# Kernel tuning notes

Measured on AMD Instinct MI355X. Metric: run time of the kernel, lower is better.

## Reference

```python
import jax, jax.numpy as jnp
import numpy as np

NUM_IT = 3

def squash(s):
    # squash along last (caps_dim) axis: |s|^2/(1+|s|^2) * s/|s|
    sq = jnp.sum(s * s, axis=-1, keepdims=True)
    return sq / (1.0 + sq) * (s / jnp.sqrt(sq))

def setup_inputs() -> dict:
    key = jax.random.key(0)
    k1, k2 = jax.random.split(key)
    prim_caps = jax.random.normal(k1, (256, 1152, 8), dtype=jnp.float32)
    W = jax.random.normal(k2, (1, 1152, 10, 16, 8), dtype=jnp.float32)
    return {"prim_caps": prim_caps, "W": W}

def reference(prim_caps, W):
    # u_hat[b,r,c,d] = W[0,r,c,d,i] @ prim_caps[b,r,i]
    u_hat = jnp.einsum('rcdi,bri->brcd', W[0], prim_caps)
    R, C = W.shape[1], W.shape[2]
    b_ij = jnp.zeros((R, C), dtype=u_hat.dtype)  # logits shared across batch
    v = None
    for _ in range(NUM_IT):
        c_ij = jax.nn.softmax(b_ij, axis=1)                     # softmax over caps dim
        s = jnp.einsum('rc,brcd->bcd', c_ij, u_hat)             # weighted sum over routes
        v = squash(s)                                            # [b, caps, dim]
        # agreement <u_hat, v>, averaged over batch (matches torch mean(dim=0))
        b_ij = b_ij + jnp.einsum('brcd,bcd->brc', u_hat, v).mean(axis=0)
    return v[..., None]  # [bs, num_caps, caps_dim, 1] matching torch output
```

## Files before the change

kernel.cpp:

```cpp
#include <hip/hip_runtime.h>
#include <hip/hip_bf16.h>
#include <math.h>


typedef __bf16 bf16x8 __attribute__((ext_vector_type(8)));
typedef float v4f __attribute__((ext_vector_type(4)));

__device__ __forceinline__ float b2f(unsigned short u) {
    return __uint_as_float(((unsigned)u) << 16);
}
__device__ __forceinline__ unsigned short f2b(float f) {
    unsigned x = __float_as_uint(f);
    return (unsigned short)((x + 0x7FFFu + ((x >> 16) & 1u)) >> 16);
}
__device__ __forceinline__ void split4(float4 x, unsigned short* h, unsigned short* l) {
    const float* xf = (const float*)&x;
    #pragma unroll
    for (int i = 0; i < 4; ++i) {
        h[i] = f2b(xf[i]);
        l[i] = f2b(xf[i] - b2f(h[i]));
    }
}
__device__ __forceinline__ uint2 pack4(const unsigned short* s) {
    uint2 w;
    w.x = s[0] | ((unsigned)s[1] << 16);
    w.y = s[2] | ((unsigned)s[3] << 16);
    return w;
}
__device__ __forceinline__ uint4 pack8(const unsigned short* s) {
    uint4 w;
    w.x = s[0] | ((unsigned)s[1] << 16); w.y = s[2] | ((unsigned)s[3] << 16);
    w.z = s[4] | ((unsigned)s[5] << 16); w.w = s[6] | ((unsigned)s[7] << 16);
    return w;
}

__global__ __launch_bounds__(256) void split_pw_kernel(
    const float4* __restrict__ P4, uint4* __restrict__ PAh, uint4* __restrict__ PAl,
    uint4* __restrict__ Pth, uint4* __restrict__ Ptl,
    const float4* __restrict__ W4, uint2* __restrict__ Wh, uint2* __restrict__ Wl)
{
    __shared__ unsigned short ldsH[64 * 72];
    __shared__ unsigned short ldsL[64 * 72];
    const int tid = threadIdx.x;

    if (blockIdx.x >= 576) {
        const int idx = (blockIdx.x - 576) * 256 + tid;
        unsigned short h[4], l[4];
        split4(W4[idx], h, l);
        Wh[idx] = pack4(h);
        Wl[idx] = pack4(l);
        return;
    }

    const int b0 = (blockIdx.x & 3) * 64;
    const int k0 = (blockIdx.x >> 2) * 64;
    #pragma unroll
    for (int j = 0; j < 4; ++j) {
        int idx = tid + j * 256;
        int row = idx >> 4, col4 = idx & 15;
        int g = (b0 + row) * 2304 + (k0 >> 2) + col4;
        unsigned short h[4], l[4];
        split4(P4[g], h, l);
        #pragma unroll
        for (int i = 0; i < 4; ++i) {
            ldsH[(col4 * 4 + i) * 72 + row] = h[i];
            ldsL[(col4 * 4 + i) * 72 + row] = l[i];
        }
    }
    __syncthreads();
    #pragma unroll
    for (int j = 0; j < 2; ++j) {
        int idx = tid + j * 256;
        int lane = idx & 63, sub = idx >> 6;
        int bt = sub & 3, kkl = sub >> 1 >> 1;
        int lm = lane & 15, q = lane >> 4;
        unsigned short h[8], l[8];
        #pragma unroll
        for (int t = 0; t < 8; ++t) {
            int kl = kkl * 32 + q * 8 + t;
            int row = bt * 16 + lm;
            h[t] = ldsH[kl * 72 + row];
            l[t] = ldsL[kl * 72 + row];
        }
        size_t o = ((size_t)((blockIdx.x & 3) * 4 + bt) * 288
                    + ((blockIdx.x >> 2) * 2 + kkl)) * 64 + lane;
        PAh[o] = pack8(h);
        PAl[o] = pack8(l);
    }
    #pragma unroll
    for (int j = 0; j < 2; ++j) {
        int idx = tid + j * 256;
        int krow = idx >> 3, bcol = idx & 7;
        unsigned short h[8], l[8];
        #pragma unroll
        for (int i = 0; i < 8; ++i) {
            h[i] = ldsH[krow * 72 + bcol * 8 + i];
            l[i] = ldsL[krow * 72 + bcol * 8 + i];
        }
        Pth[(size_t)(k0 + krow) * 32 + (b0 >> 3) + bcol] = pack8(h);
        Ptl[(size_t)(k0 + krow) * 32 + (b0 >> 3) + bcol] = pack8(l);
    }
}

__global__ __launch_bounds__(512) void sgemm_kernel(
    const uint4* __restrict__ Ah, const uint4* __restrict__ Al,
    const uint4* __restrict__ Bh, const uint4* __restrict__ Bl,
    uint2* __restrict__ vth, uint2* __restrict__ vtl,
    float* __restrict__ outb, int uniform, int last)
{
    __shared__ float comb[8][64][4];
    const int tid = threadIdx.x;
    const int wave = tid >> 6, lane = tid & 63;
    const int lm = lane & 15, q = lane >> 4;
    const int xcd = blockIdx.x & 7, s0 = blockIdx.x >> 3;
    const int c = (xcd & 1) * 5 + (s0 % 5);
    const int b0 = ((xcd >> 1) * 4 + (s0 / 5)) * 16;

    const uint4* Ahp = Ah + (size_t)(b0 >> 4) * 288 * 64 + lane;
    const uint4* Alp = Al + (size_t)(b0 >> 4) * 288 * 64 + lane;
    const uint4* Bhp = Bh + ((size_t)q * 10 + c) * 16 + lm;
    const uint4* Blp = Bl + ((size_t)q * 10 + c) * 16 + lm;

    v4f acc = {0.f, 0.f, 0.f, 0.f};
    const int kk0 = wave * 36;
    for (int kk = kk0; kk < kk0 + 36; ++kk) {
        bf16x8 ah = __builtin_bit_cast(bf16x8, Ahp[(size_t)kk * 64]);
        bf16x8 al = __builtin_bit_cast(bf16x8, Alp[(size_t)kk * 64]);
        bf16x8 bh = __builtin_bit_cast(bf16x8, Bhp[(size_t)kk * 640]);
        bf16x8 bl = __builtin_bit_cast(bf16x8, Blp[(size_t)kk * 640]);
        acc = __builtin_amdgcn_mfma_f32_16x16x32_bf16(ah, bh, acc, 0, 0, 0);
        acc = __builtin_amdgcn_mfma_f32_16x16x32_bf16(ah, bl, acc, 0, 0, 0);
        acc = __builtin_amdgcn_mfma_f32_16x16x32_bf16(al, bh, acc, 0, 0, 0);
    }
    #pragma unroll
    for (int r = 0; r < 4; ++r) comb[wave][lane][r] = acc[r];
    __syncthreads();
    if (wave == 0) {
        float s[4], sq[4];
        #pragma unroll
        for (int r = 0; r < 4; ++r) {
            s[r] = 0.f;
            #pragma unroll
            for (int w = 0; w < 8; ++w) s[r] += comb[w][lane][r];
            if (uniform) s[r] *= 0.1f;
            sq[r] = s[r] * s[r];
        }
        #pragma unroll
        for (int m = 1; m < 16; m <<= 1) {
            #pragma unroll
            for (int r = 0; r < 4; ++r) sq[r] += __shfl_xor(sq[r], m);
        }
        float v[4];
        #pragma unroll
        for (int r = 0; r < 4; ++r) {
            const float n = sq[r];
            v[r] = s[r] * sqrtf(n) / (1.0f + n);
        }
        if (!last) {
            unsigned short h[4], l[4];
            #pragma unroll
            for (int r = 0; r < 4; ++r) {
                h[r] = f2b(v[r]);
                l[r] = f2b(v[r] - b2f(h[r]));
            }
            const int o = (c * 16 + lm) * 64 + (b0 >> 2) + q;
            vth[o] = pack4(h);
            vtl[o] = pack4(l);
        } else {
            #pragma unroll
            for (int r = 0; r < 4; ++r)
                outb[((b0 + q * 4 + r) * 10 + c) * 16 + lm] = v[r];
        }
    }
}

__global__ __launch_bounds__(256) void agree_kernel(
    const uint4* __restrict__ vth, const uint4* __restrict__ vtl,
    const uint4* __restrict__ Pth, const uint4* __restrict__ Ptl,
    const float* __restrict__ Wf, float* __restrict__ b_log,
    unsigned short* __restrict__ Bh, unsigned short* __restrict__ Bl, int first)
{
    __shared__ float comb2[40][4][64];
    __shared__ float G_lds[160][18];
    __shared__ float part[4][10];
    __shared__ float cl[2][10];
    const int tid = threadIdx.x;
    const int wave = tid >> 6, lane = tid & 63;
    const int lm = lane & 15, q = lane >> 4;
    const int n0 = blockIdx.x * 16;

    v4f acc[10];
    #pragma unroll
    for (int mt = 0; mt < 10; ++mt) acc[mt] = (v4f){0.f, 0.f, 0.f, 0.f};
    #pragma unroll
    for (int kx = 0; kx < 2; ++kx) {
        const int kk = wave * 2 + kx;
        bf16x8 bh_ = __builtin_bit_cast(bf16x8, Pth[(size_t)(n0 + lm) * 32 + kk * 4 + q]);
        bf16x8 bl_ = __builtin_bit_cast(bf16x8, Ptl[(size_t)(n0 + lm) * 32 + kk * 4 + q]);
        #pragma unroll
        for (int mt = 0; mt < 10; ++mt) {
            bf16x8 ah = __builtin_bit_cast(bf16x8, vth[(size_t)(mt * 16 + lm) * 32 + kk * 4 + q]);
            bf16x8 al = __builtin_bit_cast(bf16x8, vtl[(size_t)(mt * 16 + lm) * 32 + kk * 4 + q]);
            acc[mt] = __builtin_amdgcn_mfma_f32_16x16x32_bf16(ah, bh_, acc[mt], 0, 0, 0);
            acc[mt] = __builtin_amdgcn_mfma_f32_16x16x32_bf16(ah, bl_, acc[mt], 0, 0, 0);
            acc[mt] = __builtin_amdgcn_mfma_f32_16x16x32_bf16(al, bh_, acc[mt], 0, 0, 0);
        }
    }
    #pragma unroll
    for (int mt = 0; mt < 10; ++mt)
        #pragma unroll
        for (int r = 0; r < 4; ++r)
            comb2[mt * 4 + r][wave][lane] = acc[mt][r];
    __syncthreads();
    #pragma unroll
    for (int j = 0; j < 10; ++j) {
        const int c40 = wave * 10 + j;
        float s_ = comb2[c40][0][lane] + comb2[c40][1][lane]
                 + comb2[c40][2][lane] + comb2[c40][3][lane];
        const int mt = c40 >> 2, reg = c40 & 3;
        G_lds[mt * 16 + q * 4 + reg][lm] = s_;
    }
    __syncthreads();

    const int rl = tid >> 7;
    const int t = tid & 127;
    const int r = (n0 >> 3) + rl;
    const int wid2 = tid >> 6;

    float wv[10], a[10];
    #pragma unroll
    for (int c = 0; c < 10; ++c) {
        wv[c] = Wf[((size_t)r * 10 + c) * 128 + t];
        float g = G_lds[c * 16 + (t >> 3)][rl * 8 + (t & 7)];
        a[c] = wv[c] * g;
    }
    #pragma unroll
    for (int m = 1; m < 64; m <<= 1) {
        #pragma unroll
        for (int c = 0; c < 10; ++c) a[c] += __shfl_xor(a[c], m);
    }
    if (lane == 0) {
        #pragma unroll
        for (int c = 0; c < 10; ++c) part[wid2][c] = a[c];
    }
    __syncthreads();
    if (t < 10) {
        float s_ = (part[rl * 2][t] + part[rl * 2 + 1][t]) * (1.0f / 256.0f);
        float bn = (first ? 0.f : b_log[r * 10 + t]) + s_;
        b_log[r * 10 + t] = bn;
        part[rl * 2][t] = bn;
    }
    __syncthreads();
    if (t < 10) {
        float mx = part[rl * 2][0];
        #pragma unroll
        for (int j = 1; j < 10; ++j) mx = fmaxf(mx, part[rl * 2][j]);
        float den = 0.f;
        #pragma unroll
        for (int j = 0; j < 10; ++j) den += __expf(part[rl * 2][j] - mx);
        cl[rl][t] = __expf(part[rl * 2][t] - mx) / den;
    }
    __syncthreads();
    #pragma unroll
    for (int c = 0; c < 10; ++c) {
        float x = cl[rl][c] * wv[c];
        unsigned short h = f2b(x);
        Bh[((size_t)r * 10 + c) * 128 + t] = h;
        Bl[((size_t)r * 10 + c) * 128 + t] = f2b(x - b2f(h));
    }
}

extern "C" void kernel_launch(void* const* d_in, const int* in_sizes, int n_in,
                              void* d_out, int out_size, void* d_ws, size_t ws_size,
                              hipStream_t stream)
{
    const float4* P4 = (const float4*)d_in[0];
    const float4* W4 = (const float4*)d_in[1];
    char* wsb = (char*)d_ws;
    float* b_log = (float*)(wsb + 0);
    uint2* vth   = (uint2*)(wsb + 131072);
    uint2* vtl   = (uint2*)(wsb + 262144);
    uint4* PAh   = (uint4*)(wsb + 393216);
    uint4* PAl   = (uint4*)(wsb + 5242880);
    uint4* Pth   = (uint4*)(wsb + 10485760);
    uint4* Ptl   = (uint4*)(wsb + 15728640);
    uint2* Wh    = (uint2*)(wsb + 20971520);
    uint2* Wl    = (uint2*)(wsb + 25165824);
    unsigned short* Bh = (unsigned short*)(wsb + 29360128);
    unsigned short* Bl = (unsigned short*)(wsb + 33554432);
    float* outb  = (float*)d_out;
    const float* Wf = (const float*)W4;

    split_pw_kernel<<<2016, 256, 0, stream>>>(P4, PAh, PAl, Pth, Ptl, W4, Wh, Wl);

    sgemm_kernel<<<160, 512, 0, stream>>>((const uint4*)PAh, (const uint4*)PAl,
                                          (const uint4*)Wh, (const uint4*)Wl,
                                          vth, vtl, outb, 1, 0);
    agree_kernel<<<576, 256, 0, stream>>>((const uint4*)vth, (const uint4*)vtl,
                                          Pth, Ptl, Wf, b_log, Bh, Bl, 1);
    sgemm_kernel<<<160, 512, 0, stream>>>((const uint4*)PAh, (const uint4*)PAl,
                                          (const uint4*)Bh, (const uint4*)Bl,
                                          vth, vtl, outb, 0, 0);
    agree_kernel<<<576, 256, 0, stream>>>((const uint4*)vth, (const uint4*)vtl,
                                          Pth, Ptl, Wf, b_log, Bh, Bl, 0);
    sgemm_kernel<<<160, 512, 0, stream>>>((const uint4*)PAh, (const uint4*)PAl,
                                          (const uint4*)Bh, (const uint4*)Bl,
                                          vth, vtl, outb, 0, 1);
}
```

Measured before the change: 160.5 us.

## Store MFMA operands in fragment-native layout for coalesced per-lane loads

Rewrites the layouts of W split, P transpose, v, and routing-weight buffers so that each MFMA operand fragment is a contiguous 64-lane block of uint4s. The sgemm and agree kernels then load B and A fragments with stride-64 lane-contiguous addresses instead of strided gathers. Producers (split kernel, sgemm epilogue, agree epilogue) write in the new tiled order, which makes some of their stores more scattered. The goal is to cut memory transactions in the hot GEMM loops.

```diff
diff --git a/kernel.cpp b/kernel.cpp
--- a/kernel.cpp
+++ b/kernel.cpp
@@ -36,7 +36,7 @@
 
 __global__ __launch_bounds__(256) void split_pw_kernel(
     const float4* __restrict__ P4, uint4* __restrict__ PAh, uint4* __restrict__ PAl,
-    uint4* __restrict__ Pth, uint4* __restrict__ Ptl,
+    uint4* __restrict__ PTh, uint4* __restrict__ PTl,
     const float4* __restrict__ W4, uint2* __restrict__ Wh, uint2* __restrict__ Wl)
 {
     __shared__ unsigned short ldsH[64 * 72];
@@ -45,10 +45,16 @@
 
     if (blockIdx.x >= 576) {
         const int idx = (blockIdx.x - 576) * 256 + tid;
+        const int j = idx & 1;
+        const int t16 = idx >> 1;
+        const int d = t16 & 15;
+        const int rc = t16 >> 4;
+        const int cc = rc % 10, r = rc / 10;
         unsigned short h[4], l[4];
         split4(W4[idx], h, l);
-        Wh[idx] = pack4(h);
-        Wl[idx] = pack4(l);
+        const size_t f = ((size_t)cc * 288 + (r >> 2)) * 64 + (r & 3) * 16 + d;
+        Wh[f * 2 + j] = pack4(h);
+        Wl[f * 2 + j] = pack4(l);
         return;
     }
 
@@ -72,7 +78,7 @@
     for (int j = 0; j < 2; ++j) {
         int idx = tid + j * 256;
         int lane = idx & 63, sub = idx >> 6;
-        int bt = sub & 3, kkl = sub >> 1 >> 1;
+        int bt = sub & 3, kkl = sub >> 2;
         int lm = lane & 15, q = lane >> 4;
         unsigned short h[8], l[8];
         #pragma unroll
@@ -97,8 +103,12 @@
             h[i] = ldsH[krow * 72 + bcol * 8 + i];
             l[i] = ldsL[krow * 72 + bcol * 8 + i];
         }
-        Pth[(size_t)(k0 + krow) * 32 + (b0 >> 3) + bcol] = pack8(h);
-        Ptl[(size_t)(k0 + krow) * 32 + (b0 >> 3) + bcol] = pack8(l);
+        const int gk = k0 + krow;
+        const int gcol = (b0 >> 3) + bcol;
+        const int kk = gcol >> 2, q = gcol & 3;
+        size_t o = ((size_t)(gk >> 4) * 8 + kk) * 64 + q * 16 + (gk & 15);
+        PTh[o] = pack8(h);
+        PTl[o] = pack8(l);
     }
 }
 
@@ -118,16 +128,16 @@
 
     const uint4* Ahp = Ah + (size_t)(b0 >> 4) * 288 * 64 + lane;
     const uint4* Alp = Al + (size_t)(b0 >> 4) * 288 * 64 + lane;
-    const uint4* Bhp = Bh + ((size_t)q * 10 + c) * 16 + lm;
-    const uint4* Blp = Bl + ((size_t)q * 10 + c) * 16 + lm;
+    const uint4* Bhp = Bh + (size_t)c * 288 * 64 + lane;
+    const uint4* Blp = Bl + (size_t)c * 288 * 64 + lane;
 
     v4f acc = {0.f, 0.f, 0.f, 0.f};
     const int kk0 = wave * 36;
     for (int kk = kk0; kk < kk0 + 36; ++kk) {
         bf16x8 ah = __builtin_bit_cast(bf16x8, Ahp[(size_t)kk * 64]);
         bf16x8 al = __builtin_bit_cast(bf16x8, Alp[(size_t)kk * 64]);
-        bf16x8 bh = __builtin_bit_cast(bf16x8, Bhp[(size_t)kk * 640]);
-        bf16x8 bl = __builtin_bit_cast(bf16x8, Blp[(size_t)kk * 640]);
+        bf16x8 bh = __builtin_bit_cast(bf16x8, Bhp[(size_t)kk * 64]);
+        bf16x8 bl = __builtin_bit_cast(bf16x8, Blp[(size_t)kk * 64]);
         acc = __builtin_amdgcn_mfma_f32_16x16x32_bf16(ah, bh, acc, 0, 0, 0);
         acc = __builtin_amdgcn_mfma_f32_16x16x32_bf16(ah, bl, acc, 0, 0, 0);
         acc = __builtin_amdgcn_mfma_f32_16x16x32_bf16(al, bh, acc, 0, 0, 0);
@@ -163,9 +173,11 @@
                 h[r] = f2b(v[r]);
                 l[r] = f2b(v[r] - b2f(h[r]));
             }
-            const int o = (c * 16 + lm) * 64 + (b0 >> 2) + q;
-            vth[o] = pack4(h);
-            vtl[o] = pack4(l);
+            const int jcol = (b0 >> 2) + q;
+            const int J = jcol >> 1;
+            const size_t f = ((size_t)c * 8 + (J >> 2)) * 64 + (J & 3) * 16 + lm;
+            vth[f * 2 + (jcol & 1)] = pack4(h);
+            vtl[f * 2 + (jcol & 1)] = pack4(l);
         } else {
             #pragma unroll
             for (int r = 0; r < 4; ++r)
@@ -176,7 +188,7 @@
 
 __global__ __launch_bounds__(256) void agree_kernel(
     const uint4* __restrict__ vth, const uint4* __restrict__ vtl,
-    const uint4* __restrict__ Pth, const uint4* __restrict__ Ptl,
+    const uint4* __restrict__ PTh, const uint4* __restrict__ PTl,
     const float* __restrict__ Wf, float* __restrict__ b_log,
     unsigned short* __restrict__ Bh, unsigned short* __restrict__ Bl, int first)
 {
@@ -189,18 +201,23 @@
     const int lm = lane & 15, q = lane >> 4;
     const int n0 = blockIdx.x * 16;
 
+    const uint4* PThp = PTh + (size_t)blockIdx.x * 512 + lane;
+    const uint4* PTlp = PTl + (size_t)blockIdx.x * 512 + lane;
+    const uint4* vthp = vth + lane;
+    const uint4* vtlp = vtl + lane;
+
     v4f acc[10];
     #pragma unroll
     for (int mt = 0; mt < 10; ++mt) acc[mt] = (v4f){0.f, 0.f, 0.f, 0.f};
     #pragma unroll
     for (int kx = 0; kx < 2; ++kx) {
         const int kk = wave * 2 + kx;
-        bf16x8 bh_ = __builtin_bit_cast(bf16x8, Pth[(size_t)(n0 + lm) * 32 + kk * 4 + q]);
-        bf16x8 bl_ = __builtin_bit_cast(bf16x8, Ptl[(size_t)(n0 + lm) * 32 + kk * 4 + q]);
+        bf16x8 bh_ = __builtin_bit_cast(bf16x8, PThp[(size_t)kk * 64]);
+        bf16x8 bl_ = __builtin_bit_cast(bf16x8, PTlp[(size_t)kk * 64]);
         #pragma unroll
         for (int mt = 0; mt < 10; ++mt) {
-            bf16x8 ah = __builtin_bit_cast(bf16x8, vth[(size_t)(mt * 16 + lm) * 32 + kk * 4 + q]);
-            bf16x8 al = __builtin_bit_cast(bf16x8, vtl[(size_t)(mt * 16 + lm) * 32 + kk * 4 + q]);
+            bf16x8 ah = __builtin_bit_cast(bf16x8, vthp[(size_t)(mt * 8 + kk) * 64]);
+            bf16x8 al = __builtin_bit_cast(bf16x8, vtlp[(size_t)(mt * 8 + kk) * 64]);
             acc[mt] = __builtin_amdgcn_mfma_f32_16x16x32_bf16(ah, bh_, acc[mt], 0, 0, 0);
             acc[mt] = __builtin_amdgcn_mfma_f32_16x16x32_bf16(ah, bl_, acc[mt], 0, 0, 0);
             acc[mt] = __builtin_amdgcn_mfma_f32_16x16x32_bf16(al, bh_, acc[mt], 0, 0, 0);
@@ -265,8 +282,9 @@
     for (int c = 0; c < 10; ++c) {
         float x = cl[rl][c] * wv[c];
         unsigned short h = f2b(x);
-        Bh[((size_t)r * 10 + c) * 128 + t] = h;
-        Bl[((size_t)r * 10 + c) * 128 + t] = f2b(x - b2f(h));
+        const size_t base = ((size_t)c * 288 + (r >> 2)) * 512 + 128 * (r & 3);
+        Bh[base + t] = h;
+        Bl[base + t] = f2b(x - b2f(h));
     }
 }
 
@@ -282,8 +300,8 @@
     uint2* vtl   = (uint2*)(wsb + 262144);
     uint4* PAh   = (uint4*)(wsb + 393216);
     uint4* PAl   = (uint4*)(wsb + 5242880);
-    uint4* Pth   = (uint4*)(wsb + 10485760);
-    uint4* Ptl   = (uint4*)(wsb + 15728640);
+    uint4* PTh   = (uint4*)(wsb + 10485760);
+    uint4* PTl   = (uint4*)(wsb + 15728640);
     uint2* Wh    = (uint2*)(wsb + 20971520);
     uint2* Wl    = (uint2*)(wsb + 25165824);
     unsigned short* Bh = (unsigned short*)(wsb + 29360128);
@@ -291,18 +309,18 @@
     float* outb  = (float*)d_out;
     const float* Wf = (const float*)W4;
 
-    split_pw_kernel<<<2016, 256, 0, stream>>>(P4, PAh, PAl, Pth, Ptl, W4, Wh, Wl);
+    split_pw_kernel<<<2016, 256, 0, stream>>>(P4, PAh, PAl, PTh, PTl, W4, Wh, Wl);
 
     sgemm_kernel<<<160, 512, 0, stream>>>((const uint4*)PAh, (const uint4*)PAl,
                                           (const uint4*)Wh, (const uint4*)Wl,
                                           vth, vtl, outb, 1, 0);
     agree_kernel<<<576, 256, 0, stream>>>((const uint4*)vth, (const uint4*)vtl,
-                                          Pth, Ptl, Wf, b_log, Bh, Bl, 1);
+                                          PTh, PTl, Wf, b_log, Bh, Bl, 1);
     sgemm_kernel<<<160, 512, 0, stream>>>((const uint4*)PAh, (const uint4*)PAl,
                                           (const uint4*)Bh, (const uint4*)Bl,
                                           vth, vtl, outb, 0, 0);
     agree_kernel<<<576, 256, 0, stream>>>((const uint4*)vth, (const uint4*)vtl,
-                                          Pth, Ptl, Wf, b_log, Bh, Bl, 0);
+                                          PTh, PTl, Wf, b_log, Bh, Bl, 0);
     sgemm_kernel<<<160, 512, 0, stream>>>((const uint4*)PAh, (const uint4*)PAl,
                                           (const uint4*)Bh, (const uint4*)Bl,
                                           vth, vtl, outb, 0, 1);
```

After: 136.5 us. 15.0% less time.
